# Optimization experiments

Measured on AMD Instinct MI355X. Metric: run time of the kernel, lower is better.

Reference implementation:

```python
import jax, jax.numpy as jnp
import numpy as np

N = 50000   # num_nodes
E = 500000  # num_edges
R = 8       # relations
C = 128     # channels
B = 4       # num_bases


def setup_inputs() -> dict:
    key = jax.random.key(0)
    ks = jax.random.split(key, 12)
    inp = {
        "edge_index": jax.random.randint(ks[0], (2, E), 0, N, dtype=jnp.int64 if jax.config.jax_enable_x64 else jnp.int32),
        "edge_type": jax.random.randint(ks[1], (E,), 0, R, dtype=jnp.int64 if jax.config.jax_enable_x64 else jnp.int32),
        "basis1": jax.random.normal(ks[2], (B, N, C), jnp.float32) * 0.02,
        "comp1": jax.random.normal(ks[3], (R, B), jnp.float32) * 0.5,
        "root1": jax.random.normal(ks[4], (N, C), jnp.float32) * 0.02,
        "bias1": jnp.zeros((C,), jnp.float32),
        "basis_b0": jax.random.normal(ks[5], (B, C, C), jnp.float32) * 0.05,
        "comp_b0": jax.random.normal(ks[6], (R, B), jnp.float32) * 0.5,
        "root_b0": jax.random.normal(ks[7], (C, C), jnp.float32) * 0.05,
        "bias_b0": jnp.zeros((C,), jnp.float32),
        "basis_b1": jax.random.normal(ks[8], (B, 2 * C, C), jnp.float32) * 0.05,
        "comp_b1": jax.random.normal(ks[9], (R, B), jnp.float32) * 0.5,
        "root_b1": jax.random.normal(ks[10], (2 * C, C), jnp.float32) * 0.05,
        "bias_b1": jnp.zeros((C,), jnp.float32),
    }
    return inp


def _mean_scatter(msg, mask, dst):
    # per-relation mean aggregation at destination nodes
    s = jax.ops.segment_sum(msg, dst, num_segments=N)          # [N, C]
    cnt = jax.ops.segment_sum(mask, dst, num_segments=N)       # [N]
    return s / jnp.maximum(cnt, 1.0)[:, None]


def _rgcn_first(edge_index, edge_type, basis, comp, root, bias):
    # x is None: one-hot node features -> transformed features are weight rows
    src, dst = edge_index[0], edge_index[1]
    agg = jnp.zeros((N, C), basis.dtype)
    for r in range(R):
        hr = jnp.einsum('b,bnc->nc', comp[r], basis)           # [N, C] relation-r weight rows
        mask = (edge_type == r).astype(basis.dtype)            # [E]
        msg = hr[src] * mask[:, None]                          # gather + mask
        agg = agg + _mean_scatter(msg, mask, dst)
    return jax.nn.relu(agg + root + bias)


def _rgcn_layer(x, edge_index, edge_type, basis, comp, root, bias):
    src, dst = edge_index[0], edge_index[1]
    agg = jnp.zeros((N, C), x.dtype)
    for r in range(R):
        Wr = jnp.einsum('b,bic->ic', comp[r], basis)           # [in, C]
        hr = x @ Wr                                            # [N, C]
        mask = (edge_type == r).astype(x.dtype)
        msg = hr[src] * mask[:, None]
        agg = agg + _mean_scatter(msg, mask, dst)
    return jax.nn.relu(agg + x @ root + bias)


def reference(edge_index, edge_type, basis1, comp1, root1, bias1,
              basis_b0, comp_b0, root_b0, bias_b0,
              basis_b1, comp_b1, root_b1, bias_b1):
    h = _rgcn_first(edge_index, edge_type, basis1, comp1, root1, bias1)       # [N, C]
    h = jnp.concatenate([h, _rgcn_layer(h, edge_index, edge_type, basis_b0, comp_b0, root_b0, bias_b0)], axis=1)  # [N, 2C]
    h = jnp.concatenate([h, _rgcn_layer(h, edge_index, edge_type, basis_b1, comp_b1, root_b1, bias_b1)], axis=1)  # [N, 3C]
    return jax.nn.log_softmax(h, axis=1)
```

## Files before the change

kernel.cpp:

```cpp
#include <hip/hip_runtime.h>
#include <cstdint>
#include <cstddef>

#define NN 50000
#define EE 500000
#define RR 8
#define CC 128
#define BB 4
#define H3C 384
#define NB 196
#define YS 64.0f
#define YSI (1.0f / 64.0f)

typedef unsigned short ushort_t;
typedef __bf16 bf16x8 __attribute__((ext_vector_type(8)));
typedef float f32x4 __attribute__((ext_vector_type(4)));
typedef float f32x2 __attribute__((ext_vector_type(2)));
typedef unsigned short u16x8 __attribute__((ext_vector_type(8)));

static __device__ __forceinline__ ushort_t f2bf(float f) {
  unsigned u = __float_as_uint(f);
  unsigned r = (u + 0x7fffu + ((u >> 16) & 1u)) >> 16;
  return (ushort_t)r;
}
static __device__ __forceinline__ float bf2f(ushort_t u) {
  return __uint_as_float(((unsigned)u) << 16);
}

__global__ void zero_int_k(int* p, int n) {
  int i = blockIdx.x * 256 + threadIdx.x;
  if (i < n) p[i] = 0;
}

__global__ void count_k(const int* __restrict__ ei, const int* __restrict__ et, int* cnt) {
  int e = blockIdx.x * 256 + threadIdx.x;
  if (e >= EE) return;
  int d = ei[EE + e];
  int r = et[e];
  atomicAdd(&cnt[r * NN + d], 1);
}

__global__ __launch_bounds__(256) void scanA_k(const int* __restrict__ cnt_rd, int* off, int* bsum) {
  __shared__ int s[256];
  int t = threadIdx.x;
  int i = blockIdx.x * 256 + t;
  int v = 0;
  if (i < NN) {
#pragma unroll
    for (int r = 0; r < RR; ++r) v += cnt_rd[r * NN + i];
  }
  s[t] = v;
  __syncthreads();
  for (int d = 1; d < 256; d <<= 1) {
    int x = (t >= d) ? s[t - d] : 0;
    __syncthreads();
    s[t] += x;
    __syncthreads();
  }
  if (i < NN) off[i] = s[t] - v;
  if (t == 255) bsum[blockIdx.x] = s[255];
}

__global__ __launch_bounds__(256) void scanB_k(const int* __restrict__ bsum, int* bbase) {
  __shared__ int s[256];
  int t = threadIdx.x;
  int v = (t < NB) ? bsum[t] : 0;
  s[t] = v;
  __syncthreads();
  for (int d = 1; d < 256; d <<= 1) {
    int x = (t >= d) ? s[t - d] : 0;
    __syncthreads();
    s[t] += x;
    __syncthreads();
  }
  if (t < NB) bbase[t] = s[t] - v;
}

__global__ void scanC_k(int* off, const int* __restrict__ bbase) {
  int i = blockIdx.x * 256 + threadIdx.x;
  if (i < NN) off[i] += bbase[i >> 8];
  if (i == 0) off[NN] = EE;
}

__global__ void fill_k(const int* __restrict__ ei, const int* __restrict__ et,
                       const int* __restrict__ cnt_rd, const int* __restrict__ off,
                       int* cur, uint2* __restrict__ payload) {
  int e = blockIdx.x * 256 + threadIdx.x;
  if (e >= EE) return;
  int s = ei[e], d = ei[EE + e], r = et[e];
  int pos = off[d] + atomicAdd(&cur[d], 1);
  float w = 1.0f / (float)max(cnt_rd[r * NN + d], 1);
  payload[pos] = make_uint2((unsigned)s | ((unsigned)r << 20), __float_as_uint(w));
}

__global__ void makebasisq_k(const float* __restrict__ basis1, unsigned char* __restrict__ yq) {
  int u = blockIdx.x * 256 + threadIdx.x;
  if (u >= NN * 128) return;
  int n = u >> 7, q = u & 127;
  int b = q >> 5, c0 = (q & 31) * 4;
  float4 v = *(const float4*)(basis1 + ((size_t)b * NN + n) * CC + c0);
  int pk = __builtin_amdgcn_cvt_pk_fp8_f32(v.x * YS, v.y * YS, 0, false);
  pk = __builtin_amdgcn_cvt_pk_fp8_f32(v.z * YS, v.w * YS, pk, true);
  *(unsigned*)(yq + (size_t)n * 512 + b * 128 + c0) = (unsigned)pk;
}

__global__ __launch_bounds__(256) void aggry_k(const int* __restrict__ off,
                                               const uint2* __restrict__ payload,
                                               const unsigned char* __restrict__ yq,
                                               const float* __restrict__ comp,
                                               const float* __restrict__ rootsrc,
                                               const float* __restrict__ bias,
                                               ushort_t* __restrict__ xbw, int xoff) {
  __shared__ float comps[RR * BB];
  if (threadIdx.x < RR * BB) comps[threadIdx.x] = comp[threadIdx.x] * YSI;
  __syncthreads();
  int wave = threadIdx.x >> 6, lane = threadIdx.x & 63;
  int d = blockIdx.x * 4 + wave;
  if (d >= NN) return;
  int beg = off[d], end = off[d + 1];
  int half = lane >> 5, l = lane & 31;
  float a0 = 0.f, a1 = 0.f, a2 = 0.f, a3 = 0.f;
  for (int i = beg + half; i < end; i += 2) {
    uint2 p = payload[i];
    const unsigned char* row = yq + (size_t)(p.x & 0xFFFFFu) * 512 + l * 4;
    unsigned u0 = *(const unsigned*)row;
    unsigned u1 = *(const unsigned*)(row + 128);
    unsigned u2 = *(const unsigned*)(row + 256);
    unsigned u3 = *(const unsigned*)(row + 384);
    float w = __uint_as_float(p.y);
    int r4 = (int)(p.x >> 20) * BB;
    float w0 = w * comps[r4 + 0], w1 = w * comps[r4 + 1];
    float w2 = w * comps[r4 + 2], w3 = w * comps[r4 + 3];
    f32x2 lo = __builtin_amdgcn_cvt_pk_f32_fp8(u0, false);
    f32x2 hi = __builtin_amdgcn_cvt_pk_f32_fp8(u0, true);
    a0 += w0 * lo.x; a1 += w0 * lo.y; a2 += w0 * hi.x; a3 += w0 * hi.y;
    lo = __builtin_amdgcn_cvt_pk_f32_fp8(u1, false);
    hi = __builtin_amdgcn_cvt_pk_f32_fp8(u1, true);
    a0 += w1 * lo.x; a1 += w1 * lo.y; a2 += w1 * hi.x; a3 += w1 * hi.y;
    lo = __builtin_amdgcn_cvt_pk_f32_fp8(u2, false);
    hi = __builtin_amdgcn_cvt_pk_f32_fp8(u2, true);
    a0 += w2 * lo.x; a1 += w2 * lo.y; a2 += w2 * hi.x; a3 += w2 * hi.y;
    lo = __builtin_amdgcn_cvt_pk_f32_fp8(u3, false);
    hi = __builtin_amdgcn_cvt_pk_f32_fp8(u3, true);
    a0 += w3 * lo.x; a1 += w3 * lo.y; a2 += w3 * hi.x; a3 += w3 * hi.y;
  }
  a0 += __shfl_xor(a0, 32);
  a1 += __shfl_xor(a1, 32);
  a2 += __shfl_xor(a2, 32);
  a3 += __shfl_xor(a3, 32);
  if (half == 0) {
    int c = l * 4;
    float4 rt = *(const float4*)(rootsrc + (size_t)d * CC + c);
    float4 bs = *(const float4*)(bias + c);
    float v0 = fmaxf(a0 + rt.x + bs.x, 0.f);
    float v1 = fmaxf(a1 + rt.y + bs.y, 0.f);
    float v2 = fmaxf(a2 + rt.z + bs.z, 0.f);
    float v3 = fmaxf(a3 + rt.w + bs.w, 0.f);
    ushort_t pk[4] = {f2bf(v0), f2bf(v1), f2bf(v2), f2bf(v3)};
    *(uint2*)(xbw + (size_t)d * 256 + xoff + c) = *(const uint2*)pk;
  }
}

__global__ __launch_bounds__(256) void aggrsm_k(const int* __restrict__ off,
                                                const uint2* __restrict__ payload,
                                                const unsigned char* __restrict__ yq,
                                                const float* __restrict__ comp,
                                                const float* __restrict__ rootsrc,
                                                const float* __restrict__ bias,
                                                const ushort_t* __restrict__ xb,
                                                float* __restrict__ out) {
  __shared__ float comps[RR * BB];
  if (threadIdx.x < RR * BB) comps[threadIdx.x] = comp[threadIdx.x] * YSI;
  __syncthreads();
  int wave = threadIdx.x >> 6, lane = threadIdx.x & 63;
  int d = blockIdx.x * 4 + wave;
  if (d >= NN) return;
  int beg = off[d], end = off[d + 1];
  int half = lane >> 5, l = lane & 31;
  float a0 = 0.f, a1 = 0.f, a2 = 0.f, a3 = 0.f;
  for (int i = beg + half; i < end; i += 2) {
    uint2 p = payload[i];
    const unsigned char* row = yq + (size_t)(p.x & 0xFFFFFu) * 512 + l * 4;
    unsigned u0 = *(const unsigned*)row;
    unsigned u1 = *(const unsigned*)(row + 128);
    unsigned u2 = *(const unsigned*)(row + 256);
    unsigned u3 = *(const unsigned*)(row + 384);
    float w = __uint_as_float(p.y);
    int r4 = (int)(p.x >> 20) * BB;
    float w0 = w * comps[r4 + 0], w1 = w * comps[r4 + 1];
    float w2 = w * comps[r4 + 2], w3 = w * comps[r4 + 3];
    f32x2 lo = __builtin_amdgcn_cvt_pk_f32_fp8(u0, false);
    f32x2 hi = __builtin_amdgcn_cvt_pk_f32_fp8(u0, true);
    a0 += w0 * lo.x; a1 += w0 * lo.y; a2 += w0 * hi.x; a3 += w0 * hi.y;
    lo = __builtin_amdgcn_cvt_pk_f32_fp8(u1, false);
    hi = __builtin_amdgcn_cvt_pk_f32_fp8(u1, true);
    a0 += w1 * lo.x; a1 += w1 * lo.y; a2 += w1 * hi.x; a3 += w1 * hi.y;
    lo = __builtin_amdgcn_cvt_pk_f32_fp8(u2, false);
    hi = __builtin_amdgcn_cvt_pk_f32_fp8(u2, true);
    a0 += w2 * lo.x; a1 += w2 * lo.y; a2 += w2 * hi.x; a3 += w2 * hi.y;
    lo = __builtin_amdgcn_cvt_pk_f32_fp8(u3, false);
    hi = __builtin_amdgcn_cvt_pk_f32_fp8(u3, true);
    a0 += w3 * lo.x; a1 += w3 * lo.y; a2 += w3 * hi.x; a3 += w3 * hi.y;
  }
  a0 += __shfl_xor(a0, 32);
  a1 += __shfl_xor(a1, 32);
  a2 += __shfl_xor(a2, 32);
  a3 += __shfl_xor(a3, 32);
  int c0 = (lane & 31) * 4;
  float4 rt = *(const float4*)(rootsrc + (size_t)d * CC + c0);
  float4 bs = *(const float4*)(bias + c0);
  float h0 = fmaxf(a0 + rt.x + bs.x, 0.f);
  float h1 = fmaxf(a1 + rt.y + bs.y, 0.f);
  float h2 = fmaxf(a2 + rt.z + bs.z, 0.f);
  float h3v = fmaxf(a3 + rt.w + bs.w, 0.f);
  float vals[6];
#pragma unroll
  for (int jj = 0; jj < 4; ++jj)
    vals[jj] = bf2f(xb[(size_t)d * 256 + jj * 64 + lane]);
  int s4 = lane >> 2, e = lane & 3;
  {
    float b0 = __shfl(h0, s4), b1 = __shfl(h1, s4), b2 = __shfl(h2, s4), b3 = __shfl(h3v, s4);
    float x01 = (e & 1) ? b1 : b0, x23 = (e & 1) ? b3 : b2;
    vals[4] = (e & 2) ? x23 : x01;
  }
  {
    int s5 = 16 + s4;
    float b0 = __shfl(h0, s5), b1 = __shfl(h1, s5), b2 = __shfl(h2, s5), b3 = __shfl(h3v, s5);
    float x01 = (e & 1) ? b1 : b0, x23 = (e & 1) ? b3 : b2;
    vals[5] = (e & 2) ? x23 : x01;
  }
  float m = vals[0];
#pragma unroll
  for (int jj = 1; jj < 6; ++jj) m = fmaxf(m, vals[jj]);
#pragma unroll
  for (int o = 32; o > 0; o >>= 1) m = fmaxf(m, __shfl_xor(m, o));
  float ssum = 0.f;
#pragma unroll
  for (int jj = 0; jj < 6; ++jj) ssum += expf(vals[jj] - m);
#pragma unroll
  for (int o = 32; o > 0; o >>= 1) ssum += __shfl_xor(ssum, o);
  float ls = logf(ssum);
#pragma unroll
  for (int jj = 0; jj < 6; ++jj)
    out[(size_t)d * H3C + jj * 64 + lane] = vals[jj] - m - ls;
}

template <int K_IN>
__global__ void makew5_k(const float* __restrict__ basis, const float* __restrict__ root,
                         ushort_t* __restrict__ Wt) {
  int f = blockIdx.x * 256 + threadIdx.x;
  constexpr int KD = K_IN / 32;
  int tot = 5 * KD * 8 * 64;
  if (f >= tot) return;
  int l = f & 63;
  int fi = f >> 6;
  int cb = fi & 7;
  int rem = fi >> 3;
  int kk = rem & (KD - 1);
  int s = rem / KD;
  int fr = l & 15, fq = l >> 4;
  int c = cb * 16 + fr;
  int k0 = kk * 32 + fq * 8;
  ushort_t o[8];
#pragma unroll
  for (int j = 0; j < 8; ++j) {
    int k = k0 + j;
    float v = (s < 4) ? basis[((size_t)s * K_IN + k) * CC + c]
                      : root[(size_t)k * CC + c];
    o[j] = f2bf(v);
  }
  *(u16x8*)(Wt + (size_t)f * 8) = *(const u16x8*)o;
}

template <int K_IN>
__global__ __launch_bounds__(256) void gemmy_k(const ushort_t* __restrict__ xb,
                                               const ushort_t* __restrict__ Wt,
                                               unsigned char* __restrict__ yq,
                                               float* __restrict__ yroot) {
  constexpr int NSTEPS = K_IN / 64;
  constexpr int XST = 72;
  __shared__ char smem[64 * 132 * 4];
  ushort_t* xs = (ushort_t*)smem;
  ushort_t* wls = (ushort_t*)(smem + 64 * XST * 2);
  int t = threadIdx.x;
  int wave = t >> 6, lane = t & 63;
  int wr = wave >> 1, wc = wave & 1;
  int fr = lane & 15, fq = lane >> 4;
  int row0 = blockIdx.x * 64;
  int s = blockIdx.y;
  const ushort_t* wslot = Wt + (size_t)s * (K_IN * 128);

  u16x8 areg0, areg1, breg[4];
  auto stage = [&](int step) {
    int seg = t & 7;
    int row = t >> 3;
    int gr = row0 + row;
    if (gr >= NN) gr = NN - 1;
    areg0 = *(const u16x8*)(xb + (size_t)gr * 256 + step * 64 + seg * 8);
    row = (t + 256) >> 3;
    gr = row0 + row;
    if (gr >= NN) gr = NN - 1;
    areg1 = *(const u16x8*)(xb + (size_t)gr * 256 + step * 64 + seg * 8);
    const ushort_t* bsrc = wslot + (size_t)step * 8192;
#pragma unroll
    for (int q = 0; q < 4; ++q)
      breg[q] = *(const u16x8*)(bsrc + (size_t)(t + q * 256) * 8);
  };

  f32x4 acc[2][4];
#pragma unroll
  for (int rf = 0; rf < 2; ++rf)
#pragma unroll
    for (int cb = 0; cb < 4; ++cb) acc[rf][cb] = (f32x4){0.f, 0.f, 0.f, 0.f};

  stage(0);
  for (int step = 0; step < NSTEPS; ++step) {
    __syncthreads();
    {
      int seg = t & 7;
      *(u16x8*)(xs + (t >> 3) * XST + seg * 8) = areg0;
      *(u16x8*)(xs + ((t + 256) >> 3) * XST + seg * 8) = areg1;
    }
#pragma unroll
    for (int q = 0; q < 4; ++q)
      *(u16x8*)(wls + (size_t)(t + q * 256) * 8) = breg[q];
    __syncthreads();
    if (step + 1 < NSTEPS) stage(step + 1);
#pragma unroll
    for (int kk = 0; kk < 2; ++kk) {
      bf16x8 a0 = *(const bf16x8*)(xs + (wr * 32 + fr) * XST + kk * 32 + fq * 8);
      bf16x8 a1 = *(const bf16x8*)(xs + (wr * 32 + 16 + fr) * XST + kk * 32 + fq * 8);
#pragma unroll
      for (int cb = 0; cb < 4; ++cb) {
        bf16x8 b = *(const bf16x8*)(wls + ((kk * 8 + wc * 4 + cb) * 64 + lane) * 8);
        acc[0][cb] = __builtin_amdgcn_mfma_f32_16x16x32_bf16(a0, b, acc[0][cb], 0, 0, 0);
        acc[1][cb] = __builtin_amdgcn_mfma_f32_16x16x32_bf16(a1, b, acc[1][cb], 0, 0, 0);
      }
    }
  }

  if (s == 4) {
#pragma unroll
    for (int rf = 0; rf < 2; ++rf)
#pragma unroll
      for (int cb = 0; cb < 4; ++cb) {
        int c = wc * 64 + cb * 16 + fr;
#pragma unroll
        for (int j = 0; j < 4; ++j) {
          int n = row0 + wr * 32 + rf * 16 + fq * 4 + j;
          if (n < NN) yroot[(size_t)n * CC + c] = acc[rf][cb][j];
        }
      }
  } else {
    __syncthreads();
    float* rp = (float*)smem;
#pragma unroll
    for (int rf = 0; rf < 2; ++rf)
#pragma unroll
      for (int cb = 0; cb < 4; ++cb)
#pragma unroll
        for (int j = 0; j < 4; ++j)
          rp[(wr * 32 + rf * 16 + fq * 4 + j) * 132 + wc * 64 + cb * 16 + fr] = acc[rf][cb][j];
    __syncthreads();
    int row = t & 63, c0 = (t >> 6) * 32;
    int gr = row0 + row;
    if (gr < NN) {
      const float* src = rp + row * 132 + c0;
      unsigned ub[8];
#pragma unroll
      for (int q = 0; q < 8; ++q) {
        float4 v = *(const float4*)(src + q * 4);
        int pk = __builtin_amdgcn_cvt_pk_fp8_f32(v.x * YS, v.y * YS, 0, false);
        pk = __builtin_amdgcn_cvt_pk_fp8_f32(v.z * YS, v.w * YS, pk, true);
        ub[q] = (unsigned)pk;
      }
      unsigned char* dst = yq + (size_t)gr * 512 + s * 128 + c0;
      *(uint4*)dst = make_uint4(ub[0], ub[1], ub[2], ub[3]);
      *(uint4*)(dst + 16) = make_uint4(ub[4], ub[5], ub[6], ub[7]);
    }
  }
}

extern "C" void kernel_launch(void* const* d_in, const int* in_sizes, int n_in,
                              void* d_out, int out_size, void* d_ws, size_t ws_size,
                              hipStream_t stream) {
  const int* ei = (const int*)d_in[0];
  const int* et = (const int*)d_in[1];
  const float* basis1 = (const float*)d_in[2];
  const float* comp1 = (const float*)d_in[3];
  const float* root1 = (const float*)d_in[4];
  const float* bias1 = (const float*)d_in[5];
  const float* basis_b0 = (const float*)d_in[6];
  const float* comp_b0 = (const float*)d_in[7];
  const float* root_b0 = (const float*)d_in[8];
  const float* bias_b0 = (const float*)d_in[9];
  const float* basis_b1 = (const float*)d_in[10];
  const float* comp_b1 = (const float*)d_in[11];
  const float* root_b1 = (const float*)d_in[12];
  const float* bias_b1 = (const float*)d_in[13];
  float* out = (float*)d_out;
  char* ws = (char*)d_ws;

  uint2* payload = (uint2*)ws;
  float* yroot = (float*)(payload + EE);
  ushort_t* xb = (ushort_t*)(yroot + (size_t)NN * CC);
  ushort_t* wt = xb + (size_t)NN * 256;
  unsigned char* yq = (unsigned char*)(wt + 327680);
  int* cnt_rd = (int*)(yq + (size_t)NN * 512);
  int* cur = cnt_rd + (size_t)RR * NN;
  int* off = cur + NN;
  int* bsum = off + NN + 1;
  int* bbase = bsum + 256;
  size_t need = (size_t)((char*)(bbase + 256) - ws);
  if (ws_size < need) return;

  zero_int_k<<<(RR * NN + NN + 255) / 256, 256, 0, stream>>>(cnt_rd, RR * NN + NN);
  count_k<<<(EE + 255) / 256, 256, 0, stream>>>(ei, et, cnt_rd);
  scanA_k<<<NB, 256, 0, stream>>>(cnt_rd, off, bsum);
  scanB_k<<<1, 256, 0, stream>>>(bsum, bbase);
  scanC_k<<<NB, 256, 0, stream>>>(off, bbase);
  fill_k<<<(EE + 255) / 256, 256, 0, stream>>>(ei, et, cnt_rd, off, cur, payload);

  const int AG_BLKS = (NN + 3) / 4;
  const int GE_BLKS = (NN + 63) / 64;
  dim3 gy(GE_BLKS, 5);

  makebasisq_k<<<(NN * 128 + 255) / 256, 256, 0, stream>>>(basis1, yq);
  aggry_k<<<AG_BLKS, 256, 0, stream>>>(off, payload, yq, comp1, root1, bias1, xb, 0);

  makew5_k<128><<<(5 * 4 * 8 * 64 + 255) / 256, 256, 0, stream>>>(basis_b0, root_b0, wt);
  gemmy_k<128><<<gy, 256, 0, stream>>>(xb, wt, yq, yroot);
  aggry_k<<<AG_BLKS, 256, 0, stream>>>(off, payload, yq, comp_b0, yroot, bias_b0, xb, CC);

  makew5_k<256><<<(5 * 8 * 8 * 64 + 255) / 256, 256, 0, stream>>>(basis_b1, root_b1, wt);
  gemmy_k<256><<<gy, 256, 0, stream>>>(xb, wt, yq, yroot);
  aggrsm_k<<<AG_BLKS, 256, 0, stream>>>(off, payload, yq, comp_b1, yroot, bias_b1, xb, out);
}
```

Baseline: 304.4 us.

## Precompute per-relation fp8 feature tables so aggregation gathers one row per edge

Instead of gathering four basis rows per edge and combining them with relation coefficients inside the aggregation loop, new kernels first materialize per-relation transformed features (R×N×C fp8) from the basis projections. The aggregation kernels then gather a single 128-byte row per edge and apply only the edge weight, with the fp8 scale folded in at the end. The edge loop is also unrolled by two to keep more loads in flight. This trades extra precompute passes and a larger workspace (R×N×C bytes written each layer) for a quarter of the gather traffic and less per-edge arithmetic. It also adds an extra fp8 rounding step after the combination in layers 2 and 3.

Result: faster. 283.1 us (-7.0%).

```diff
diff --git a/kernel.cpp b/kernel.cpp
--- a/kernel.cpp
+++ b/kernel.cpp
@@ -93,126 +93,158 @@
   payload[pos] = make_uint2((unsigned)s | ((unsigned)r << 20), __float_as_uint(w));
 }
 
-__global__ void makebasisq_k(const float* __restrict__ basis1, unsigned char* __restrict__ yq) {
-  int u = blockIdx.x * 256 + threadIdx.x;
-  if (u >= NN * 128) return;
-  int n = u >> 7, q = u & 127;
-  int b = q >> 5, c0 = (q & 31) * 4;
-  float4 v = *(const float4*)(basis1 + ((size_t)b * NN + n) * CC + c0);
-  int pk = __builtin_amdgcn_cvt_pk_fp8_f32(v.x * YS, v.y * YS, 0, false);
-  pk = __builtin_amdgcn_cvt_pk_fp8_f32(v.z * YS, v.w * YS, pk, true);
-  *(unsigned*)(yq + (size_t)n * 512 + b * 128 + c0) = (unsigned)pk;
-}
-
-__global__ __launch_bounds__(256) void aggry_k(const int* __restrict__ off,
+__global__ void makehr1q_k(const float* __restrict__ basis1, const float* __restrict__ comp1,
+                           unsigned char* __restrict__ hrq) {
+  __shared__ float comps[RR * BB];
+  if (threadIdx.x < RR * BB) comps[threadIdx.x] = comp1[threadIdx.x] * YS;
+  __syncthreads();
+  int idx = blockIdx.x * 256 + threadIdx.x;
+  if (idx >= NN * 32) return;
+  int n = idx >> 5, c0 = (idx & 31) * 4;
+  float4 y[BB];
+#pragma unroll
+  for (int b = 0; b < BB; ++b)
+    y[b] = *(const float4*)(basis1 + ((size_t)b * NN + n) * CC + c0);
+#pragma unroll
+  for (int r = 0; r < RR; ++r) {
+    float k0 = comps[r * BB + 0], k1 = comps[r * BB + 1];
+    float k2 = comps[r * BB + 2], k3 = comps[r * BB + 3];
+    float v0 = k0 * y[0].x + k1 * y[1].x + k2 * y[2].x + k3 * y[3].x;
+    float v1 = k0 * y[0].y + k1 * y[1].y + k2 * y[2].y + k3 * y[3].y;
+    float v2 = k0 * y[0].z + k1 * y[1].z + k2 * y[2].z + k3 * y[3].z;
+    float v3 = k0 * y[0].w + k1 * y[1].w + k2 * y[2].w + k3 * y[3].w;
+    int pk = __builtin_amdgcn_cvt_pk_fp8_f32(v0, v1, 0, false);
+    pk = __builtin_amdgcn_cvt_pk_fp8_f32(v2, v3, pk, true);
+    *(unsigned*)(hrq + ((size_t)r * NN + n) * CC + c0) = (unsigned)pk;
+  }
+}
+
+__global__ void makehrq_k(const unsigned char* __restrict__ yq, const float* __restrict__ comp,
+                          unsigned char* __restrict__ hrq) {
+  __shared__ float comps[RR * BB];
+  if (threadIdx.x < RR * BB) comps[threadIdx.x] = comp[threadIdx.x];
+  __syncthreads();
+  int idx = blockIdx.x * 256 + threadIdx.x;
+  if (idx >= NN * 32) return;
+  int n = idx >> 5, c0 = (idx & 31) * 4;
+  const unsigned char* yr = yq + (size_t)n * 512 + c0;
+  float y[BB][4];
+#pragma unroll
+  for (int b = 0; b < BB; ++b) {
+    unsigned u = *(const unsigned*)(yr + b * 128);
+    f32x2 lo = __builtin_amdgcn_cvt_pk_f32_fp8(u, false);
+    f32x2 hi = __builtin_amdgcn_cvt_pk_f32_fp8(u, true);
+    y[b][0] = lo.x; y[b][1] = lo.y; y[b][2] = hi.x; y[b][3] = hi.y;
+  }
+#pragma unroll
+  for (int r = 0; r < RR; ++r) {
+    float k0 = comps[r * BB + 0], k1 = comps[r * BB + 1];
+    float k2 = comps[r * BB + 2], k3 = comps[r * BB + 3];
+    float v0 = k0 * y[0][0] + k1 * y[1][0] + k2 * y[2][0] + k3 * y[3][0];
+    float v1 = k0 * y[0][1] + k1 * y[1][1] + k2 * y[2][1] + k3 * y[3][1];
+    float v2 = k0 * y[0][2] + k1 * y[1][2] + k2 * y[2][2] + k3 * y[3][2];
+    float v3 = k0 * y[0][3] + k1 * y[1][3] + k2 * y[2][3] + k3 * y[3][3];
+    int pk = __builtin_amdgcn_cvt_pk_fp8_f32(v0, v1, 0, false);
+    pk = __builtin_amdgcn_cvt_pk_fp8_f32(v2, v3, pk, true);
+    *(unsigned*)(hrq + ((size_t)r * NN + n) * CC + c0) = (unsigned)pk;
+  }
+}
+
+__global__ __launch_bounds__(256) void aggrq_k(const int* __restrict__ off,
                                                const uint2* __restrict__ payload,
-                                               const unsigned char* __restrict__ yq,
-                                               const float* __restrict__ comp,
+                                               const unsigned char* __restrict__ hrq,
                                                const float* __restrict__ rootsrc,
                                                const float* __restrict__ bias,
                                                ushort_t* __restrict__ xbw, int xoff) {
-  __shared__ float comps[RR * BB];
-  if (threadIdx.x < RR * BB) comps[threadIdx.x] = comp[threadIdx.x] * YSI;
-  __syncthreads();
   int wave = threadIdx.x >> 6, lane = threadIdx.x & 63;
   int d = blockIdx.x * 4 + wave;
   if (d >= NN) return;
   int beg = off[d], end = off[d + 1];
   int half = lane >> 5, l = lane & 31;
+  int c0 = l * 4;
   float a0 = 0.f, a1 = 0.f, a2 = 0.f, a3 = 0.f;
-  for (int i = beg + half; i < end; i += 2) {
+  int i = beg + half;
+  for (; i + 2 < end; i += 4) {
+    uint2 pA = payload[i], pB = payload[i + 2];
+    unsigned uA = *(const unsigned*)(hrq + ((size_t)(pA.x >> 20) * NN + (pA.x & 0xFFFFFu)) * CC + c0);
+    unsigned uB = *(const unsigned*)(hrq + ((size_t)(pB.x >> 20) * NN + (pB.x & 0xFFFFFu)) * CC + c0);
+    float wA = __uint_as_float(pA.y), wB = __uint_as_float(pB.y);
+    f32x2 lo = __builtin_amdgcn_cvt_pk_f32_fp8(uA, false);
+    f32x2 hi = __builtin_amdgcn_cvt_pk_f32_fp8(uA, true);
+    a0 += wA * lo.x; a1 += wA * lo.y; a2 += wA * hi.x; a3 += wA * hi.y;
+    lo = __builtin_amdgcn_cvt_pk_f32_fp8(uB, false);
+    hi = __builtin_amdgcn_cvt_pk_f32_fp8(uB, true);
+    a0 += wB * lo.x; a1 += wB * lo.y; a2 += wB * hi.x; a3 += wB * hi.y;
+  }
+  if (i < end) {
     uint2 p = payload[i];
-    const unsigned char* row = yq + (size_t)(p.x & 0xFFFFFu) * 512 + l * 4;
-    unsigned u0 = *(const unsigned*)row;
-    unsigned u1 = *(const unsigned*)(row + 128);
-    unsigned u2 = *(const unsigned*)(row + 256);
-    unsigned u3 = *(const unsigned*)(row + 384);
+    unsigned u = *(const unsigned*)(hrq + ((size_t)(p.x >> 20) * NN + (p.x & 0xFFFFFu)) * CC + c0);
     float w = __uint_as_float(p.y);
-    int r4 = (int)(p.x >> 20) * BB;
-    float w0 = w * comps[r4 + 0], w1 = w * comps[r4 + 1];
-    float w2 = w * comps[r4 + 2], w3 = w * comps[r4 + 3];
-    f32x2 lo = __builtin_amdgcn_cvt_pk_f32_fp8(u0, false);
-    f32x2 hi = __builtin_amdgcn_cvt_pk_f32_fp8(u0, true);
-    a0 += w0 * lo.x; a1 += w0 * lo.y; a2 += w0 * hi.x; a3 += w0 * hi.y;
-    lo = __builtin_amdgcn_cvt_pk_f32_fp8(u1, false);
-    hi = __builtin_amdgcn_cvt_pk_f32_fp8(u1, true);
-    a0 += w1 * lo.x; a1 += w1 * lo.y; a2 += w1 * hi.x; a3 += w1 * hi.y;
-    lo = __builtin_amdgcn_cvt_pk_f32_fp8(u2, false);
-    hi = __builtin_amdgcn_cvt_pk_f32_fp8(u2, true);
-    a0 += w2 * lo.x; a1 += w2 * lo.y; a2 += w2 * hi.x; a3 += w2 * hi.y;
-    lo = __builtin_amdgcn_cvt_pk_f32_fp8(u3, false);
-    hi = __builtin_amdgcn_cvt_pk_f32_fp8(u3, true);
-    a0 += w3 * lo.x; a1 += w3 * lo.y; a2 += w3 * hi.x; a3 += w3 * hi.y;
+    f32x2 lo = __builtin_amdgcn_cvt_pk_f32_fp8(u, false);
+    f32x2 hi = __builtin_amdgcn_cvt_pk_f32_fp8(u, true);
+    a0 += w * lo.x; a1 += w * lo.y; a2 += w * hi.x; a3 += w * hi.y;
   }
   a0 += __shfl_xor(a0, 32);
   a1 += __shfl_xor(a1, 32);
   a2 += __shfl_xor(a2, 32);
   a3 += __shfl_xor(a3, 32);
   if (half == 0) {
-    int c = l * 4;
-    float4 rt = *(const float4*)(rootsrc + (size_t)d * CC + c);
-    float4 bs = *(const float4*)(bias + c);
-    float v0 = fmaxf(a0 + rt.x + bs.x, 0.f);
-    float v1 = fmaxf(a1 + rt.y + bs.y, 0.f);
-    float v2 = fmaxf(a2 + rt.z + bs.z, 0.f);
-    float v3 = fmaxf(a3 + rt.w + bs.w, 0.f);
+    float4 rt = *(const float4*)(rootsrc + (size_t)d * CC + c0);
+    float4 bs = *(const float4*)(bias + c0);
+    float v0 = fmaxf(a0 * YSI + rt.x + bs.x, 0.f);
+    float v1 = fmaxf(a1 * YSI + rt.y + bs.y, 0.f);
+    float v2 = fmaxf(a2 * YSI + rt.z + bs.z, 0.f);
+    float v3 = fmaxf(a3 * YSI + rt.w + bs.w, 0.f);
     ushort_t pk[4] = {f2bf(v0), f2bf(v1), f2bf(v2), f2bf(v3)};
-    *(uint2*)(xbw + (size_t)d * 256 + xoff + c) = *(const uint2*)pk;
-  }
-}
-
-__global__ __launch_bounds__(256) void aggrsm_k(const int* __restrict__ off,
-                                                const uint2* __restrict__ payload,
-                                                const unsigned char* __restrict__ yq,
-                                                const float* __restrict__ comp,
-                                                const float* __restrict__ rootsrc,
-                                                const float* __restrict__ bias,
-                                                const ushort_t* __restrict__ xb,
-                                                float* __restrict__ out) {
-  __shared__ float comps[RR * BB];
-  if (threadIdx.x < RR * BB) comps[threadIdx.x] = comp[threadIdx.x] * YSI;
-  __syncthreads();
+    *(uint2*)(xbw + (size_t)d * 256 + xoff + c0) = *(const uint2*)pk;
+  }
+}
+
+__global__ __launch_bounds__(256) void aggrsmq_k(const int* __restrict__ off,
+                                                 const uint2* __restrict__ payload,
+                                                 const unsigned char* __restrict__ hrq,
+                                                 const float* __restrict__ rootsrc,
+                                                 const float* __restrict__ bias,
+                                                 const ushort_t* __restrict__ xb,
+                                                 float* __restrict__ out) {
   int wave = threadIdx.x >> 6, lane = threadIdx.x & 63;
   int d = blockIdx.x * 4 + wave;
   if (d >= NN) return;
   int beg = off[d], end = off[d + 1];
   int half = lane >> 5, l = lane & 31;
+  int c0 = l * 4;
   float a0 = 0.f, a1 = 0.f, a2 = 0.f, a3 = 0.f;
-  for (int i = beg + half; i < end; i += 2) {
+  int i = beg + half;
+  for (; i + 2 < end; i += 4) {
+    uint2 pA = payload[i], pB = payload[i + 2];
+    unsigned uA = *(const unsigned*)(hrq + ((size_t)(pA.x >> 20) * NN + (pA.x & 0xFFFFFu)) * CC + c0);
+    unsigned uB = *(const unsigned*)(hrq + ((size_t)(pB.x >> 20) * NN + (pB.x & 0xFFFFFu)) * CC + c0);
+    float wA = __uint_as_float(pA.y), wB = __uint_as_float(pB.y);
+    f32x2 lo = __builtin_amdgcn_cvt_pk_f32_fp8(uA, false);
+    f32x2 hi = __builtin_amdgcn_cvt_pk_f32_fp8(uA, true);
+    a0 += wA * lo.x; a1 += wA * lo.y; a2 += wA * hi.x; a3 += wA * hi.y;
+    lo = __builtin_amdgcn_cvt_pk_f32_fp8(uB, false);
+    hi = __builtin_amdgcn_cvt_pk_f32_fp8(uB, true);
+    a0 += wB * lo.x; a1 += wB * lo.y; a2 += wB * hi.x; a3 += wB * hi.y;
+  }
+  if (i < end) {
     uint2 p = payload[i];
-    const unsigned char* row = yq + (size_t)(p.x & 0xFFFFFu) * 512 + l * 4;
-    unsigned u0 = *(const unsigned*)row;
-    unsigned u1 = *(const unsigned*)(row + 128);
-    unsigned u2 = *(const unsigned*)(row + 256);
-    unsigned u3 = *(const unsigned*)(row + 384);
+    unsigned u = *(const unsigned*)(hrq + ((size_t)(p.x >> 20) * NN + (p.x & 0xFFFFFu)) * CC + c0);
     float w = __uint_as_float(p.y);
-    int r4 = (int)(p.x >> 20) * BB;
-    float w0 = w * comps[r4 + 0], w1 = w * comps[r4 + 1];
-    float w2 = w * comps[r4 + 2], w3 = w * comps[r4 + 3];
-    f32x2 lo = __builtin_amdgcn_cvt_pk_f32_fp8(u0, false);
-    f32x2 hi = __builtin_amdgcn_cvt_pk_f32_fp8(u0, true);
-    a0 += w0 * lo.x; a1 += w0 * lo.y; a2 += w0 * hi.x; a3 += w0 * hi.y;
-    lo = __builtin_amdgcn_cvt_pk_f32_fp8(u1, false);
-    hi = __builtin_amdgcn_cvt_pk_f32_fp8(u1, true);
-    a0 += w1 * lo.x; a1 += w1 * lo.y; a2 += w1 * hi.x; a3 += w1 * hi.y;
-    lo = __builtin_amdgcn_cvt_pk_f32_fp8(u2, false);
-    hi = __builtin_amdgcn_cvt_pk_f32_fp8(u2, true);
-    a0 += w2 * lo.x; a1 += w2 * lo.y; a2 += w2 * hi.x; a3 += w2 * hi.y;
-    lo = __builtin_amdgcn_cvt_pk_f32_fp8(u3, false);
-    hi = __builtin_amdgcn_cvt_pk_f32_fp8(u3, true);
-    a0 += w3 * lo.x; a1 += w3 * lo.y; a2 += w3 * hi.x; a3 += w3 * hi.y;
+    f32x2 lo = __builtin_amdgcn_cvt_pk_f32_fp8(u, false);
+    f32x2 hi = __builtin_amdgcn_cvt_pk_f32_fp8(u, true);
+    a0 += w * lo.x; a1 += w * lo.y; a2 += w * hi.x; a3 += w * hi.y;
   }
   a0 += __shfl_xor(a0, 32);
   a1 += __shfl_xor(a1, 32);
   a2 += __shfl_xor(a2, 32);
   a3 += __shfl_xor(a3, 32);
-  int c0 = (lane & 31) * 4;
   float4 rt = *(const float4*)(rootsrc + (size_t)d * CC + c0);
   float4 bs = *(const float4*)(bias + c0);
-  float h0 = fmaxf(a0 + rt.x + bs.x, 0.f);
-  float h1 = fmaxf(a1 + rt.y + bs.y, 0.f);
-  float h2 = fmaxf(a2 + rt.z + bs.z, 0.f);
-  float h3v = fmaxf(a3 + rt.w + bs.w, 0.f);
+  float h0 = fmaxf(a0 * YSI + rt.x + bs.x, 0.f);
+  float h1 = fmaxf(a1 * YSI + rt.y + bs.y, 0.f);
+  float h2 = fmaxf(a2 * YSI + rt.z + bs.z, 0.f);
+  float h3v = fmaxf(a3 * YSI + rt.w + bs.w, 0.f);
   float vals[6];
 #pragma unroll
   for (int jj = 0; jj < 4; ++jj)
@@ -406,7 +438,8 @@
   ushort_t* xb = (ushort_t*)(yroot + (size_t)NN * CC);
   ushort_t* wt = xb + (size_t)NN * 256;
   unsigned char* yq = (unsigned char*)(wt + 327680);
-  int* cnt_rd = (int*)(yq + (size_t)NN * 512);
+  unsigned char* hrq = yq + (size_t)NN * 512;
+  int* cnt_rd = (int*)(hrq + (size_t)RR * NN * CC);
   int* cur = cnt_rd + (size_t)RR * NN;
   int* off = cur + NN;
   int* bsum = off + NN + 1;
@@ -422,17 +455,20 @@
   fill_k<<<(EE + 255) / 256, 256, 0, stream>>>(ei, et, cnt_rd, off, cur, payload);
 
   const int AG_BLKS = (NN + 3) / 4;
+  const int HQ_BLKS = (NN * 32 + 255) / 256;
   const int GE_BLKS = (NN + 63) / 64;
   dim3 gy(GE_BLKS, 5);
 
-  makebasisq_k<<<(NN * 128 + 255) / 256, 256, 0, stream>>>(basis1, yq);
-  aggry_k<<<AG_BLKS, 256, 0, stream>>>(off, payload, yq, comp1, root1, bias1, xb, 0);
+  makehr1q_k<<<HQ_BLKS, 256, 0, stream>>>(basis1, comp1, hrq);
+  aggrq_k<<<AG_BLKS, 256, 0, stream>>>(off, payload, hrq, root1, bias1, xb, 0);
 
   makew5_k<128><<<(5 * 4 * 8 * 64 + 255) / 256, 256, 0, stream>>>(basis_b0, root_b0, wt);
   gemmy_k<128><<<gy, 256, 0, stream>>>(xb, wt, yq, yroot);
-  aggry_k<<<AG_BLKS, 256, 0, stream>>>(off, payload, yq, comp_b0, yroot, bias_b0, xb, CC);
+  makehrq_k<<<HQ_BLKS, 256, 0, stream>>>(yq, comp_b0, hrq);
+  aggrq_k<<<AG_BLKS, 256, 0, stream>>>(off, payload, hrq, yroot, bias_b0, xb, CC);
 
   makew5_k<256><<<(5 * 8 * 8 * 64 + 255) / 256, 256, 0, stream>>>(basis_b1, root_b1, wt);
   gemmy_k<256><<<gy, 256, 0, stream>>>(xb, wt, yq, yroot);
-  aggrsm_k<<<AG_BLKS, 256, 0, stream>>>(off, payload, yq, comp_b1, yroot, bias_b1, xb, out);
-}
+  makehrq_k<<<HQ_BLKS, 256, 0, stream>>>(yq, comp_b1, hrq);
+  aggrsmq_k<<<AG_BLKS, 256, 0, stream>>>(off, payload, hrq, yroot, bias_b1, xb, out);
+}
```
